# Optimization experiments

Measured on AMD Instinct MI355X. Metric: run time of the kernel, lower is better.

Reference implementation:

```python
import jax, jax.numpy as jnp
import numpy as np

B, N, DIM, H = 8, 1024, 1024, 8
HEAD_DIM = DIM // H
SCALE = HEAD_DIM ** -0.5  # scale_with_head=True


def setup_inputs() -> dict:
    key = jax.random.key(0)
    k1, k2, k3, k4 = jax.random.split(key, 4)
    return {
        "q": jax.random.normal(k1, (B, N, DIM), dtype=jnp.float32),
        "k": jax.random.normal(k2, (B, N, DIM), dtype=jnp.float32),
        "v": jax.random.normal(k3, (B, N, DIM), dtype=jnp.float32),
        "W_out": jax.random.normal(k4, (DIM, DIM), dtype=jnp.float32) * (DIM ** -0.5),
        "b_out": jnp.zeros((DIM,), dtype=jnp.float32),
    }


def reference(q, k, v, W_out, b_out):
    b, n, dim = q.shape
    h, d = H, dim // H
    # b n (h d) -> b h n d
    def split_heads(t):
        return t.reshape(b, n, h, d).transpose(0, 2, 1, 3)
    qh, kh, vh = split_heads(q), split_heads(k), split_heads(v)
    dots = jnp.einsum('bhid,bhjd->bhij', qh, kh) * SCALE
    attn = jax.nn.softmax(dots, axis=-1)
    out = jnp.einsum('bhij,bhjd->bhid', attn, vh)
    out = out.transpose(0, 2, 1, 3).reshape(b, n, dim)  # b h n d -> b n (h d)
    out = out @ W_out.T + b_out  # nn.Linear(dim, dim); dropout p=0 is identity
    return out, attn
```

## Files before the change

### kernel.cpp

```cpp
#include <hip/hip_runtime.h>

typedef __bf16 bf16x8 __attribute__((ext_vector_type(8)));
typedef unsigned short u16x8 __attribute__((ext_vector_type(8)));
typedef unsigned short u16x4 __attribute__((ext_vector_type(4)));
typedef float f32x4 __attribute__((ext_vector_type(4)));

#define B_    8
#define N_    1024
#define DIM_  1024
#define H_    8
#define HD_   128
#define SCALE_ 0.08838834764831845f

__device__ __forceinline__ unsigned short f2bf(float x) {
  unsigned int u = __float_as_uint(x);
  u += 0x7fffu + ((u >> 16) & 1u);
  return (unsigned short)(u >> 16);
}
__device__ __forceinline__ float bf2f(unsigned short h) {
  return __uint_as_float(((unsigned int)h) << 16);
}
__device__ __forceinline__ f32x4 mfma16(u16x8 a, u16x8 b, f32x4 c) {
  return __builtin_amdgcn_mfma_f32_16x16x32_bf16(
      __builtin_bit_cast(bf16x8, a), __builtin_bit_cast(bf16x8, b), c, 0, 0, 0);
}
__device__ __forceinline__ void gl_lds16(const void* g, void* l) {
  __builtin_amdgcn_global_load_lds(
      (const __attribute__((address_space(1))) unsigned int*)g,
      (__attribute__((address_space(3))) unsigned int*)l, 16, 0, 0);
}
#define SBAR() do { asm volatile("" ::: "memory"); __builtin_amdgcn_s_barrier(); \
                    asm volatile("" ::: "memory"); } while (0)
#define LGKM0() do { asm volatile("s_waitcnt lgkmcnt(0)" ::: "memory"); \
                     __builtin_amdgcn_sched_barrier(0); } while (0)
#define VMC(n)  asm volatile("s_waitcnt vmcnt(" #n ")" ::: "memory")

#define WS_KIMG  ((size_t)0)
#define WS_VIMG  ((size_t)32 << 20)
#define WS_WIMG  ((size_t)64 << 20)
#define WS_AOIMG ((size_t)68 << 20)

__global__ __launch_bounds__(256)
void prep_k(const float* __restrict__ gk, char* __restrict__ kimg) {
  const int blk = blockIdx.x;
  const int bh = blk >> 4, it = blk & 15;
  const int bb = bh >> 3, hh = bh & 7;
  const int t = threadIdx.x;
  char* base = kimg + (size_t)bh * 524288 + it * 32768;
  const float* src = gk + ((size_t)bb * N_ + it * 64) * DIM_ + hh * HD_;
  #pragma unroll
  for (int c = 0; c < 8; ++c) {
    const int idx = t + 256 * c;
    const int key = idx >> 5, dq = (idx & 31) * 4;
    f32x4 f = *(const f32x4*)(src + (size_t)key * DIM_ + dq);
    u16x4 h, g;
    #pragma unroll
    for (int j = 0; j < 4; ++j) {
      unsigned short hv = f2bf(f[j]);
      h[j] = hv;
      g[j] = f2bf(f[j] - bf2f(hv));
    }
    const int dh = dq >> 6, dloc = dq & 63;
    const int off = (dloc * 2) ^ ((key & 7) << 4);
    char* dst = base + dh * 16384 + key * 256;
    *(u16x4*)(dst + off) = h;
    *(u16x4*)(dst + 128 + off) = g;
  }
}

__global__ __launch_bounds__(256)
void prep_v(const float* __restrict__ gv, char* __restrict__ vimg) {
  __shared__ float tile[32][132];
  const int blk = blockIdx.x;
  const int bh = blk >> 5, kt = blk & 31;
  const int bb = bh >> 3, hh = bh & 7;
  const int t = threadIdx.x;
  const float* src = gv + ((size_t)bb * N_ + kt * 32) * DIM_ + hh * HD_;
  #pragma unroll
  for (int c = 0; c < 4; ++c) {
    const int idx = t + 256 * c;
    const int key = idx >> 5, dq = (idx & 31) * 4;
    *(f32x4*)&tile[key][dq] = *(const f32x4*)(src + (size_t)key * DIM_ + dq);
  }
  __syncthreads();
  char* base = vimg + (size_t)bh * 524288 + kt * 16384;
  #pragma unroll
  for (int c = 0; c < 2; ++c) {
    const int oc = t + 256 * c;
    const int d = oc >> 2, kc = oc & 3;
    u16x8 h, g;
    #pragma unroll
    for (int j = 0; j < 8; ++j) {
      float x = tile[kc * 8 + j][d];
      unsigned short hv = f2bf(x);
      h[j] = hv;
      g[j] = f2bf(x - bf2f(hv));
    }
    const int off = (d * 64 + kc * 16) ^ ((d & 7) << 4);
    *(u16x8*)(base + off) = h;
    *(u16x8*)(base + 8192 + off) = g;
  }
}

__global__ __launch_bounds__(256)
void prep_w(const float* __restrict__ gw, char* __restrict__ wimg) {
  const int idx = blockIdx.x * 256 + threadIdx.x;
  const int row = idx >> 7, c0 = (idx & 127) * 8;
  const float* s = gw + (size_t)row * DIM_ + c0;
  f32x4 f0 = *(const f32x4*)s;
  f32x4 f1 = *(const f32x4*)(s + 4);
  u16x8 h, g;
  #pragma unroll
  for (int j = 0; j < 8; ++j) {
    float x = j < 4 ? f0[j] : f1[j - 4];
    unsigned short hv = f2bf(x);
    h[j] = hv;
    g[j] = f2bf(x - bf2f(hv));
  }
  const int nt = row >> 6, rl = row & 63;
  const int st = c0 >> 5, kl = c0 & 31;
  char* base = wimg + ((size_t)(nt * 32 + st) * 64 + rl) * 128;
  const int swz = (rl & 7) << 4;
  *(u16x8*)(base + ((kl * 2) ^ swz)) = h;
  *(u16x8*)(base + ((64 + kl * 2) ^ swz)) = g;
}

struct K1Smem {
  unsigned short p[64 * 1024];
  union {
    char kb[2][16384];
    char vt[2][16384];
    struct { char pad[16384]; float partial[4][64]; float rinv[64]; } pp;
  } u;
};

__global__ __launch_bounds__(1024, 4)
void attn_kernel(const float* __restrict__ gq, const char* __restrict__ kimg,
                 const char* __restrict__ vimg, float* __restrict__ gattn,
                 char* __restrict__ aoimg) {
  __shared__ K1Smem sm;
  const int bid = blockIdx.x;
  const int xcd = bid & 7, slot = bid >> 3;
  const int bh = xcd + 8 * (slot >> 4);
  const int qt = slot & 15;
  const int bb = bh >> 3, hh = bh & 7;

  const int tid = threadIdx.x;
  const int wid = tid >> 6, lane = tid & 63;
  const int rg = wid >> 2;
  const int kg = wid & 3;
  const int l15 = lane & 15, l4 = lane >> 4;

  const char* kimg_bh = kimg + (size_t)bh * 524288;
  const char* vimg_bh = vimg + (size_t)bh * 524288;

  auto issueK = [&](int s) {
    const char* src = kimg_bh + s * 16384 + wid * 1024 + lane * 16;
    gl_lds16(src, sm.u.kb[s & 1] + wid * 1024);
  };
  auto issueV = [&](int kt) {
    const char* src = vimg_bh + kt * 16384 + wid * 1024 + lane * 16;
    gl_lds16(src, sm.u.vt[kt & 1] + wid * 1024);
  };

  issueK(0);

  u16x8 qhi[4], qlo[4];
  {
    const int qrow = qt * 64 + rg * 16 + l15;
    const float* qp = gq + ((size_t)bb * N_ + qrow) * DIM_ + hh * HD_;
    #pragma unroll
    for (int t = 0; t < 4; ++t) {
      const int d0 = t * 32 + l4 * 8;
      f32x4 f0 = *(const f32x4*)(qp + d0);
      f32x4 f1 = *(const f32x4*)(qp + d0 + 4);
      #pragma unroll
      for (int j = 0; j < 8; ++j) {
        float x = (j < 4 ? f0[j] : f1[j - 4]) * SCALE_;
        unsigned short hi = f2bf(x);
        qhi[t][j] = hi;
        qlo[t][j] = f2bf(x - bf2f(hi));
      }
    }
  }

  issueK(1);
  VMC(1);
  SBAR();

  float lsum = 0.f;
  const int key16 = kg * 16 + l15;
  const int kswz = (key16 & 7) << 4;
  const char* krow0 = sm.u.kb[0] + key16 * 256;
  const char* krow1 = sm.u.kb[1] + key16 * 256;
  const int prow_i = rg * 16 + l15;
  char* const prow = (char*)sm.p + prow_i * 2048;
  const int pswz = (prow_i & 7) << 4;

  f32x4 a0, a1, a2;
  #pragma unroll 2
  for (int s = 0; s < 32; ++s) {
    const int dh = s & 1;
    if (s >= 1 && s < 31) issueK(s + 1);
    else if (s == 31) issueV(0);
    const char* krow = dh ? krow1 : krow0;
    u16x8 khi[2], klo[2];
    #pragma unroll
    for (int tl = 0; tl < 2; ++tl) {
      const int off = (tl * 64 + l4 * 16) ^ kswz;
      khi[tl] = *(const u16x8*)(krow + off);
      klo[tl] = *(const u16x8*)(krow + 128 + off);
    }
    if (dh == 0) {
      a0 = f32x4{0.f, 0.f, 0.f, 0.f};
      a1 = f32x4{0.f, 0.f, 0.f, 0.f};
      a2 = f32x4{0.f, 0.f, 0.f, 0.f};
    }
    __builtin_amdgcn_s_setprio(1);
    #pragma unroll
    for (int tl = 0; tl < 2; ++tl) {
      const int t = dh * 2 + tl;
      a0 = mfma16(khi[tl], qhi[t], a0);
      a1 = mfma16(klo[tl], qhi[t], a1);
      a2 = mfma16(khi[tl], qlo[t], a2);
    }
    __builtin_amdgcn_s_setprio(0);
    if (dh == 1) {
      const int keyb = ((s >> 1) * 64 + kg * 16 + l4 * 4) * 2;
      u16x4 pk;
      float ls = 0.f;
      #pragma unroll
      for (int r = 0; r < 4; ++r) {
        float sv = (a0[r] + a1[r]) + a2[r];
        sv = fminf(sv, 60.0f);
        float p = __expf(sv);
        ls += p;
        pk[r] = f2bf(p);
      }
      lsum += ls;
      *(u16x4*)(prow + (keyb ^ pswz)) = pk;
    }
    if (s < 31) VMC(0);
    SBAR();
  }

  {
    float s0 = lsum;
    s0 += __shfl_xor(s0, 16);
    s0 += __shfl_xor(s0, 32);
    if (lane < 16) sm.u.pp.partial[kg][rg * 16 + lane] = s0;
  }
  LGKM0();
  SBAR();
  if (tid < 64) {
    float t4 = sm.u.pp.partial[0][tid] + sm.u.pp.partial[1][tid] +
               sm.u.pp.partial[2][tid] + sm.u.pp.partial[3][tid];
    sm.u.pp.rinv[tid] = 1.0f / t4;
  }
  LGKM0();
  SBAR();
  float rvf[4];
  #pragma unroll
  for (int r = 0; r < 4; ++r)
    rvf[r] = sm.u.pp.rinv[rg * 16 + l4 * 4 + r];
  const bool writer = (kg == 0);
  float rvw = 0.f;
  if (writer) rvw = sm.u.pp.rinv[prow_i];
  LGKM0();
  VMC(0);
  SBAR();

  f32x4 oacc[2];
  oacc[0] = f32x4{0.f, 0.f, 0.f, 0.f};
  oacc[1] = f32x4{0.f, 0.f, 0.f, 0.f};

  float* arow = nullptr;
  if (writer)
    arow = gattn + ((size_t)bh * N_ + qt * 64 + prow_i) * N_ + l4 * 8;

  #pragma unroll 2
  for (int kt = 0; kt < 32; ++kt) {
    if (kt < 31) issueV(kt + 1);
    const char* vbase = sm.u.vt[kt & 1];
    u16x8 vh[2], vl[2];
    #pragma unroll
    for (int ct = 0; ct < 2; ++ct) {
      const int d = kg * 32 + ct * 16 + l15;
      const int off = (d * 64 + l4 * 16) ^ ((d & 7) << 4);
      vh[ct] = *(const u16x8*)(vbase + off);
      vl[ct] = *(const u16x8*)(vbase + 8192 + off);
    }
    u16x8 pa = *(const u16x8*)(prow + ((kt * 64 + l4 * 16) ^ pswz));
    __builtin_amdgcn_s_setprio(1);
    #pragma unroll
    for (int ct = 0; ct < 2; ++ct) {
      oacc[ct] = mfma16(pa, vh[ct], oacc[ct]);
      oacc[ct] = mfma16(pa, vl[ct], oacc[ct]);
    }
    __builtin_amdgcn_s_setprio(0);
    if (writer) {
      f32x4 o0, o1;
      o0[0] = bf2f(pa[0]) * rvw; o0[1] = bf2f(pa[1]) * rvw;
      o0[2] = bf2f(pa[2]) * rvw; o0[3] = bf2f(pa[3]) * rvw;
      o1[0] = bf2f(pa[4]) * rvw; o1[1] = bf2f(pa[5]) * rvw;
      o1[2] = bf2f(pa[6]) * rvw; o1[3] = bf2f(pa[7]) * rvw;
      __builtin_nontemporal_store(o0, (f32x4*)(arow + kt * 32));
      __builtin_nontemporal_store(o1, (f32x4*)(arow + kt * 32 + 4));
    }
    LGKM0();
    if (kt < 31) {
      if (writer) { VMC(2); }
      else        { VMC(0); }
    }
    SBAR();
  }

  {
    char* aobase = aoimg + ((size_t)((bb * 16 + qt) * 32 + hh * 4 + kg)) * 8192;
    #pragma unroll
    for (int ct = 0; ct < 2; ++ct) {
      const int colloc = ct * 16 + l15;
      #pragma unroll
      for (int r = 0; r < 4; ++r) {
        const int rl = rg * 16 + l4 * 4 + r;
        const int swz = (rl & 7) << 4;
        float val = oacc[ct][r] * rvf[r];
        unsigned short hv = f2bf(val);
        unsigned short lv = f2bf(val - bf2f(hv));
        char* rp = aobase + rl * 128;
        __builtin_nontemporal_store(hv, (unsigned short*)(rp + ((colloc * 2) ^ swz)));
        __builtin_nontemporal_store(lv, (unsigned short*)(rp + ((64 + colloc * 2) ^ swz)));
      }
    }
  }
}

struct K2Smem {
  char A[2][8192];
  char Bm[2][8192];
};

__global__ __launch_bounds__(512)
void proj_kernel(const char* __restrict__ aoimg, const char* __restrict__ wimg,
                 const float* __restrict__ gbias, float* __restrict__ gout) {
  __shared__ K2Smem sm;
  const int orig = blockIdx.x;
  const int xcd = orig & 7, idx = orig >> 3;
  const int nt = xcd * 2 + (idx >> 7);
  const int mt = idx & 127;
  const int tid = threadIdx.x;
  const int wid = tid >> 6, lane = tid & 63;
  const int wr = wid >> 2, wc = wid & 3;
  const int l15 = lane & 15, l4 = lane >> 4;

  auto issue = [&](int s) {
    const char* sa = aoimg + ((size_t)(mt * 32 + s)) * 8192 + wid * 1024 + lane * 16;
    gl_lds16(sa, sm.A[s & 1] + wid * 1024);
    const char* sb = wimg + ((size_t)(nt * 32 + s)) * 8192 + wid * 1024 + lane * 16;
    gl_lds16(sb, sm.Bm[s & 1] + wid * 1024);
  };

  f32x4 acc[2];
  acc[0] = f32x4{0.f, 0.f, 0.f, 0.f};
  acc[1] = f32x4{0.f, 0.f, 0.f, 0.f};

  issue(0);
  VMC(0);
  SBAR();
  #pragma unroll 2
  for (int s = 0; s < 32; ++s) {
    if (s < 31) issue(s + 1);
    const char* Ab = sm.A[s & 1];
    const char* Bb = sm.Bm[s & 1];
    u16x8 ah[2], al[2], bh, bl;
    #pragma unroll
    for (int t = 0; t < 2; ++t) {
      const int row = wr * 32 + t * 16 + l15;
      const char* rp = Ab + row * 128;
      const int swz = (row & 7) << 4;
      ah[t] = *(const u16x8*)(rp + ((l4 * 16) ^ swz));
      al[t] = *(const u16x8*)(rp + ((64 + l4 * 16) ^ swz));
    }
    {
      const int col = wc * 16 + l15;
      const char* rp = Bb + col * 128;
      const int swz = (col & 7) << 4;
      bh = *(const u16x8*)(rp + ((l4 * 16) ^ swz));
      bl = *(const u16x8*)(rp + ((64 + l4 * 16) ^ swz));
    }
    __builtin_amdgcn_s_setprio(1);
    #pragma unroll
    for (int i = 0; i < 2; ++i) {
      acc[i] = mfma16(ah[i], bh, acc[i]);
      acc[i] = mfma16(ah[i], bl, acc[i]);
      acc[i] = mfma16(al[i], bh, acc[i]);
    }
    __builtin_amdgcn_s_setprio(0);
    LGKM0();
    if (s < 31) VMC(0);
    SBAR();
  }

  const int col = nt * 64 + wc * 16 + l15;
  const float bv = gbias[col];
  #pragma unroll
  for (int i = 0; i < 2; ++i) {
    float* dst = gout + (size_t)(mt * 64 + wr * 32 + i * 16 + l4 * 4) * DIM_ + col;
    #pragma unroll
    for (int r = 0; r < 4; ++r)
      dst[(size_t)r * DIM_] = acc[i][r] + bv;
  }
}

extern "C" void kernel_launch(void* const* d_in, const int* in_sizes, int n_in,
                              void* d_out, int out_size, void* d_ws, size_t ws_size,
                              hipStream_t stream) {
  const float* q    = (const float*)d_in[0];
  const float* k    = (const float*)d_in[1];
  const float* v    = (const float*)d_in[2];
  const float* W    = (const float*)d_in[3];
  const float* bias = (const float*)d_in[4];
  float* out  = (float*)d_out;
  float* attn = out + (size_t)B_ * N_ * DIM_;

  char* ws = (char*)d_ws;
  char* kimg  = ws + WS_KIMG;
  char* vimg  = ws + WS_VIMG;
  char* wimg  = ws + WS_WIMG;
  char* aoimg = ws + WS_AOIMG;

  prep_k<<<64 * 16, 256, 0, stream>>>(k, kimg);
  prep_v<<<64 * 32, 256, 0, stream>>>(v, vimg);
  prep_w<<<512, 256, 0, stream>>>(W, wimg);
  attn_kernel<<<B_ * H_ * (N_ / 64), 1024, 0, stream>>>(q, kimg, vimg, attn, aoimg);
  proj_kernel<<<2048, 512, 0, stream>>>(aoimg, wimg, bias, out);
}
```

Measured before the change: 278.1 us.

## Merge prep kernels, use 32x32 MFMA for PV, enlarge projection tiles

Merges the three prep kernels into one launch. The attention PV phase moves to 32x32x16 MFMA, with waves split across key halves and a cross-wave LDS reduction; the V image layout changes to match. The projection GEMM goes from 64x64 to 128x128 tiles per block with a 4x2 accumulator grid per wave, raising operand reuse and cutting grid size. The costs are more register pressure, an extra barrier and reduction in the attention epilogue, and fewer, larger blocks in the projection.

Result: slower. 317.4 us (+14.1%).

```diff
diff --git a/kernel.cpp b/kernel.cpp
--- a/kernel.cpp
+++ b/kernel.cpp
@@ -4,6 +4,7 @@
 typedef unsigned short u16x8 __attribute__((ext_vector_type(8)));
 typedef unsigned short u16x4 __attribute__((ext_vector_type(4)));
 typedef float f32x4 __attribute__((ext_vector_type(4)));
+typedef float f32x16 __attribute__((ext_vector_type(16)));
 
 #define B_    8
 #define N_    1024
@@ -24,6 +25,10 @@
   return __builtin_amdgcn_mfma_f32_16x16x32_bf16(
       __builtin_bit_cast(bf16x8, a), __builtin_bit_cast(bf16x8, b), c, 0, 0, 0);
 }
+__device__ __forceinline__ f32x16 mfma32(u16x8 a, u16x8 b, f32x16 c) {
+  return __builtin_amdgcn_mfma_f32_32x32x16_bf16(
+      __builtin_bit_cast(bf16x8, a), __builtin_bit_cast(bf16x8, b), c, 0, 0, 0);
+}
 __device__ __forceinline__ void gl_lds16(const void* g, void* l) {
   __builtin_amdgcn_global_load_lds(
       (const __attribute__((address_space(1))) unsigned int*)g,
@@ -41,95 +46,96 @@
 #define WS_AOIMG ((size_t)68 << 20)
 
 __global__ __launch_bounds__(256)
-void prep_k(const float* __restrict__ gk, char* __restrict__ kimg) {
+void prep_all(const float* __restrict__ gk, const float* __restrict__ gv,
+              const float* __restrict__ gw, char* __restrict__ kimg,
+              char* __restrict__ vimg, char* __restrict__ wimg) {
   const int blk = blockIdx.x;
-  const int bh = blk >> 4, it = blk & 15;
-  const int bb = bh >> 3, hh = bh & 7;
   const int t = threadIdx.x;
-  char* base = kimg + (size_t)bh * 524288 + it * 32768;
-  const float* src = gk + ((size_t)bb * N_ + it * 64) * DIM_ + hh * HD_;
-  #pragma unroll
-  for (int c = 0; c < 8; ++c) {
-    const int idx = t + 256 * c;
-    const int key = idx >> 5, dq = (idx & 31) * 4;
-    f32x4 f = *(const f32x4*)(src + (size_t)key * DIM_ + dq);
-    u16x4 h, g;
-    #pragma unroll
-    for (int j = 0; j < 4; ++j) {
-      unsigned short hv = f2bf(f[j]);
-      h[j] = hv;
-      g[j] = f2bf(f[j] - bf2f(hv));
-    }
-    const int dh = dq >> 6, dloc = dq & 63;
-    const int off = (dloc * 2) ^ ((key & 7) << 4);
-    char* dst = base + dh * 16384 + key * 256;
-    *(u16x4*)(dst + off) = h;
-    *(u16x4*)(dst + 128 + off) = g;
-  }
-}
-
-__global__ __launch_bounds__(256)
-void prep_v(const float* __restrict__ gv, char* __restrict__ vimg) {
-  __shared__ float tile[32][132];
-  const int blk = blockIdx.x;
-  const int bh = blk >> 5, kt = blk & 31;
-  const int bb = bh >> 3, hh = bh & 7;
-  const int t = threadIdx.x;
-  const float* src = gv + ((size_t)bb * N_ + kt * 32) * DIM_ + hh * HD_;
-  #pragma unroll
-  for (int c = 0; c < 4; ++c) {
-    const int idx = t + 256 * c;
-    const int key = idx >> 5, dq = (idx & 31) * 4;
-    *(f32x4*)&tile[key][dq] = *(const f32x4*)(src + (size_t)key * DIM_ + dq);
-  }
-  __syncthreads();
-  char* base = vimg + (size_t)bh * 524288 + kt * 16384;
-  #pragma unroll
-  for (int c = 0; c < 2; ++c) {
-    const int oc = t + 256 * c;
-    const int d = oc >> 2, kc = oc & 3;
+  if (blk < 1024) {
+    const int bh = blk >> 4, it = blk & 15;
+    const int bb = bh >> 3, hh = bh & 7;
+    char* base = kimg + (size_t)bh * 524288 + it * 32768;
+    const float* src = gk + ((size_t)bb * N_ + it * 64) * DIM_ + hh * HD_;
+    #pragma unroll
+    for (int c = 0; c < 8; ++c) {
+      const int idx = t + 256 * c;
+      const int key = idx >> 5, dq = (idx & 31) * 4;
+      f32x4 f = *(const f32x4*)(src + (size_t)key * DIM_ + dq);
+      u16x4 h, g;
+      #pragma unroll
+      for (int j = 0; j < 4; ++j) {
+        unsigned short hv = f2bf(f[j]);
+        h[j] = hv;
+        g[j] = f2bf(f[j] - bf2f(hv));
+      }
+      const int dh = dq >> 6, dloc = dq & 63;
+      const int off = (dloc * 2) ^ ((key & 7) << 4);
+      char* dst = base + dh * 16384 + key * 256;
+      *(u16x4*)(dst + off) = h;
+      *(u16x4*)(dst + 128 + off) = g;
+    }
+  } else if (blk < 3072) {
+    __shared__ float tile[32][132];
+    const int b2 = blk - 1024;
+    const int bh = b2 >> 5, kt = b2 & 31;
+    const int bb = bh >> 3, hh = bh & 7;
+    const float* src = gv + ((size_t)bb * N_ + kt * 32) * DIM_ + hh * HD_;
+    #pragma unroll
+    for (int c = 0; c < 4; ++c) {
+      const int idx = t + 256 * c;
+      const int key = idx >> 5, dq = (idx & 31) * 4;
+      *(f32x4*)&tile[key][dq] = *(const f32x4*)(src + (size_t)key * DIM_ + dq);
+    }
+    __syncthreads();
+    char* base = vimg + (size_t)bh * 524288 + kt * 16384;
+    #pragma unroll
+    for (int c = 0; c < 2; ++c) {
+      const int idx = t + 256 * c;
+      const int d = idx >> 2, koct = idx & 3;
+      const int sb = koct >> 1, k8 = (koct & 1) * 8;
+      u16x8 h, g;
+      #pragma unroll
+      for (int j = 0; j < 8; ++j) {
+        float x = tile[sb * 16 + k8 + j][d];
+        unsigned short hv = f2bf(x);
+        h[j] = hv;
+        g[j] = f2bf(x - bf2f(hv));
+      }
+      const int off = d * 32 + ((k8 * 2) ^ ((d & 1) << 4));
+      char* dst = base + sb * 8192;
+      *(u16x8*)(dst + off) = h;
+      *(u16x8*)(dst + 4096 + off) = g;
+    }
+  } else {
+    const int idx = (blk - 3072) * 256 + t;
+    const int n = idx >> 7, k8 = idx & 127;
+    const int k0 = k8 * 8;
+    const float* s = gw + (size_t)n * DIM_ + k0;
+    f32x4 f0 = *(const f32x4*)s;
+    f32x4 f1 = *(const f32x4*)(s + 4);
     u16x8 h, g;
     #pragma unroll
     for (int j = 0; j < 8; ++j) {
-      float x = tile[kc * 8 + j][d];
+      float x = j < 4 ? f0[j] : f1[j - 4];
       unsigned short hv = f2bf(x);
       h[j] = hv;
       g[j] = f2bf(x - bf2f(hv));
     }
-    const int off = (d * 64 + kc * 16) ^ ((d & 7) << 4);
-    *(u16x8*)(base + off) = h;
-    *(u16x8*)(base + 8192 + off) = g;
-  }
-}
-
-__global__ __launch_bounds__(256)
-void prep_w(const float* __restrict__ gw, char* __restrict__ wimg) {
-  const int idx = blockIdx.x * 256 + threadIdx.x;
-  const int row = idx >> 7, c0 = (idx & 127) * 8;
-  const float* s = gw + (size_t)row * DIM_ + c0;
-  f32x4 f0 = *(const f32x4*)s;
-  f32x4 f1 = *(const f32x4*)(s + 4);
-  u16x8 h, g;
-  #pragma unroll
-  for (int j = 0; j < 8; ++j) {
-    float x = j < 4 ? f0[j] : f1[j - 4];
-    unsigned short hv = f2bf(x);
-    h[j] = hv;
-    g[j] = f2bf(x - bf2f(hv));
-  }
-  const int nt = row >> 6, rl = row & 63;
-  const int st = c0 >> 5, kl = c0 & 31;
-  char* base = wimg + ((size_t)(nt * 32 + st) * 64 + rl) * 128;
-  const int swz = (rl & 7) << 4;
-  *(u16x8*)(base + ((kl * 2) ^ swz)) = h;
-  *(u16x8*)(base + ((64 + kl * 2) ^ swz)) = g;
+    const int T = (n >> 7) * 32 + (k0 >> 5);
+    const int rl = n & 127, kl = k0 & 31;
+    char* base = wimg + (size_t)T * 16384 + rl * 128;
+    const int swz = (rl & 7) << 4;
+    *(u16x8*)(base + ((kl * 2) ^ swz)) = h;
+    *(u16x8*)(base + ((64 + kl * 2) ^ swz)) = g;
+  }
 }
 
 struct K1Smem {
   unsigned short p[64 * 1024];
   union {
     char kb[2][16384];
-    char vt[2][16384];
+    char vb[4][8192];
+    char comb[8][4096];
     struct { char pad[16384]; float partial[4][64]; float rinv[64]; } pp;
   } u;
 };
@@ -150,6 +156,10 @@
   const int rg = wid >> 2;
   const int kg = wid & 3;
   const int l15 = lane & 15, l4 = lane >> 4;
+  const int prg = wid >> 3;
+  const int pkg = kg;
+  const int pkh = (wid >> 2) & 1;
+  const int l31 = lane & 31, l5 = lane >> 5;
 
   const char* kimg_bh = kimg + (size_t)bh * 524288;
   const char* vimg_bh = vimg + (size_t)bh * 524288;
@@ -158,9 +168,10 @@
     const char* src = kimg_bh + s * 16384 + wid * 1024 + lane * 16;
     gl_lds16(src, sm.u.kb[s & 1] + wid * 1024);
   };
-  auto issueV = [&](int kt) {
-    const char* src = vimg_bh + kt * 16384 + wid * 1024 + lane * 16;
-    gl_lds16(src, sm.u.vt[kt & 1] + wid * 1024);
+  auto issueVpair = [&](int pairbase) {
+    const int sb = pairbase + (wid >> 3);
+    const char* src = vimg_bh + (size_t)sb * 8192 + (wid & 7) * 1024 + lane * 16;
+    gl_lds16(src, sm.u.vb[sb & 3] + (wid & 7) * 1024);
   };
 
   issueK(0);
@@ -202,7 +213,7 @@
   for (int s = 0; s < 32; ++s) {
     const int dh = s & 1;
     if (s >= 1 && s < 31) issueK(s + 1);
-    else if (s == 31) issueV(0);
+    else if (s == 31) issueVpair(0);
     const char* krow = dh ? krow1 : krow0;
     u16x8 khi[2], klo[2];
     #pragma unroll
@@ -240,7 +251,8 @@
       lsum += ls;
       *(u16x4*)(prow + (keyb ^ pswz)) = pk;
     }
-    if (s < 31) VMC(0);
+    if (s < 31) { VMC(0); }
+    else       { VMC(2); }
     SBAR();
   }
 
@@ -259,156 +271,184 @@
   }
   LGKM0();
   SBAR();
-  float rvf[4];
-  #pragma unroll
-  for (int r = 0; r < 4; ++r)
-    rvf[r] = sm.u.pp.rinv[rg * 16 + l4 * 4 + r];
-  const bool writer = (kg == 0);
-  float rvw = 0.f;
-  if (writer) rvw = sm.u.pp.rinv[prow_i];
+  const float rvw = sm.u.pp.rinv[prg * 32 + l31];
+  float rv16[16];
+  if (pkh == 0) {
+    #pragma unroll
+    for (int r = 0; r < 16; ++r) {
+      const int rowreg = (r & 3) + 8 * (r >> 2) + 4 * l5;
+      rv16[r] = sm.u.pp.rinv[prg * 32 + rowreg];
+    }
+  }
   LGKM0();
   VMC(0);
   SBAR();
 
-  f32x4 oacc[2];
-  oacc[0] = f32x4{0.f, 0.f, 0.f, 0.f};
-  oacc[1] = f32x4{0.f, 0.f, 0.f, 0.f};
-
-  float* arow = nullptr;
-  if (writer)
-    arow = gattn + ((size_t)bh * N_ + qt * 64 + prow_i) * N_ + l4 * 8;
-
-  #pragma unroll 2
-  for (int kt = 0; kt < 32; ++kt) {
-    if (kt < 31) issueV(kt + 1);
-    const char* vbase = sm.u.vt[kt & 1];
-    u16x8 vh[2], vl[2];
-    #pragma unroll
-    for (int ct = 0; ct < 2; ++ct) {
-      const int d = kg * 32 + ct * 16 + l15;
-      const int off = (d * 64 + l4 * 16) ^ ((d & 7) << 4);
-      vh[ct] = *(const u16x8*)(vbase + off);
-      vl[ct] = *(const u16x8*)(vbase + 8192 + off);
-    }
-    u16x8 pa = *(const u16x8*)(prow + ((kt * 64 + l4 * 16) ^ pswz));
+  f32x16 acc = {};
+  const char* pArow = (const char*)sm.p + (prg * 32 + l31) * 2048;
+  const int paswz = ((prg * 32 + l31) & 7) << 4;
+  float* arow = gattn + ((size_t)bh * N_ + qt * 64 + prg * 32 + l31) * N_;
+
+  #pragma unroll 1
+  for (int t = 0; t < 32; ++t) {
+    if (t < 31) issueVpair(2 * (t + 1));
+    const int s = 2 * t + pkh;
+    const char* vbase = sm.u.vb[s & 3];
+    const int d = pkg * 32 + l31;
+    const int voff = d * 32 + ((l5 * 16) ^ ((d & 1) << 4));
+    u16x8 vh = *(const u16x8*)(vbase + voff);
+    u16x8 vl = *(const u16x8*)(vbase + 4096 + voff);
+    u16x8 pa = *(const u16x8*)(pArow + ((s * 32 + l5 * 16) ^ paswz));
     __builtin_amdgcn_s_setprio(1);
-    #pragma unroll
-    for (int ct = 0; ct < 2; ++ct) {
-      oacc[ct] = mfma16(pa, vh[ct], oacc[ct]);
-      oacc[ct] = mfma16(pa, vl[ct], oacc[ct]);
-    }
+    acc = mfma32(pa, vh, acc);
+    acc = mfma32(pa, vl, acc);
     __builtin_amdgcn_s_setprio(0);
-    if (writer) {
+    const bool wr = ((t & 3) == pkg);
+    if (wr) {
       f32x4 o0, o1;
       o0[0] = bf2f(pa[0]) * rvw; o0[1] = bf2f(pa[1]) * rvw;
       o0[2] = bf2f(pa[2]) * rvw; o0[3] = bf2f(pa[3]) * rvw;
       o1[0] = bf2f(pa[4]) * rvw; o1[1] = bf2f(pa[5]) * rvw;
       o1[2] = bf2f(pa[6]) * rvw; o1[3] = bf2f(pa[7]) * rvw;
-      __builtin_nontemporal_store(o0, (f32x4*)(arow + kt * 32));
-      __builtin_nontemporal_store(o1, (f32x4*)(arow + kt * 32 + 4));
+      float* dst = arow + s * 16 + l5 * 8;
+      __builtin_nontemporal_store(o0, (f32x4*)dst);
+      __builtin_nontemporal_store(o1, (f32x4*)(dst + 4));
     }
     LGKM0();
-    if (kt < 31) {
-      if (writer) { VMC(2); }
-      else        { VMC(0); }
+    if (t < 31) {
+      if (wr) { VMC(2); }
+      else    { VMC(0); }
     }
     SBAR();
   }
 
   {
-    char* aobase = aoimg + ((size_t)((bb * 16 + qt) * 32 + hh * 4 + kg)) * 8192;
-    #pragma unroll
-    for (int ct = 0; ct < 2; ++ct) {
-      const int colloc = ct * 16 + l15;
-      #pragma unroll
-      for (int r = 0; r < 4; ++r) {
-        const int rl = rg * 16 + l4 * 4 + r;
+    char* cbase = sm.u.comb[prg * 4 + pkg] + lane * 64;
+    if (pkh == 1) {
+      #pragma unroll
+      for (int q = 0; q < 4; ++q) {
+        f32x4 v = {acc[q * 4], acc[q * 4 + 1], acc[q * 4 + 2], acc[q * 4 + 3]};
+        *(f32x4*)(cbase + q * 16) = v;
+      }
+    }
+    LGKM0();
+    SBAR();
+    if (pkh == 0) {
+      #pragma unroll
+      for (int q = 0; q < 4; ++q) {
+        f32x4 v = *(const f32x4*)(cbase + q * 16);
+        acc[q * 4] += v[0]; acc[q * 4 + 1] += v[1];
+        acc[q * 4 + 2] += v[2]; acc[q * 4 + 3] += v[3];
+      }
+      const int col5 = hh * 4 + pkg;
+      const int mt = bb * 8 + (qt >> 1);
+      char* Tbase = aoimg + ((size_t)(mt * 32 + col5)) * 16384;
+      const int klb = (l31) * 2;
+      #pragma unroll
+      for (int r = 0; r < 16; ++r) {
+        const int rowreg = (r & 3) + 8 * (r >> 2) + 4 * l5;
+        const int rl = (qt & 1) * 64 + prg * 32 + rowreg;
         const int swz = (rl & 7) << 4;
-        float val = oacc[ct][r] * rvf[r];
+        float val = acc[r] * rv16[r];
         unsigned short hv = f2bf(val);
         unsigned short lv = f2bf(val - bf2f(hv));
-        char* rp = aobase + rl * 128;
-        __builtin_nontemporal_store(hv, (unsigned short*)(rp + ((colloc * 2) ^ swz)));
-        __builtin_nontemporal_store(lv, (unsigned short*)(rp + ((64 + colloc * 2) ^ swz)));
+        char* rp = Tbase + rl * 128;
+        __builtin_nontemporal_store(hv, (unsigned short*)(rp + (klb ^ swz)));
+        __builtin_nontemporal_store(lv, (unsigned short*)(rp + ((64 + klb) ^ swz)));
       }
     }
   }
 }
 
 struct K2Smem {
-  char A[2][8192];
-  char Bm[2][8192];
+  char A[2][16384];
+  char Bm[2][16384];
 };
 
-__global__ __launch_bounds__(512)
+__global__ __launch_bounds__(512, 2)
 void proj_kernel(const char* __restrict__ aoimg, const char* __restrict__ wimg,
                  const float* __restrict__ gbias, float* __restrict__ gout) {
   __shared__ K2Smem sm;
-  const int orig = blockIdx.x;
-  const int xcd = orig & 7, idx = orig >> 3;
-  const int nt = xcd * 2 + (idx >> 7);
-  const int mt = idx & 127;
+  const int nt = blockIdx.x & 7;
+  const int mt = blockIdx.x >> 3;
   const int tid = threadIdx.x;
   const int wid = tid >> 6, lane = tid & 63;
   const int wr = wid >> 2, wc = wid & 3;
   const int l15 = lane & 15, l4 = lane >> 4;
 
   auto issue = [&](int s) {
-    const char* sa = aoimg + ((size_t)(mt * 32 + s)) * 8192 + wid * 1024 + lane * 16;
-    gl_lds16(sa, sm.A[s & 1] + wid * 1024);
-    const char* sb = wimg + ((size_t)(nt * 32 + s)) * 8192 + wid * 1024 + lane * 16;
-    gl_lds16(sb, sm.Bm[s & 1] + wid * 1024);
+    const char* sa = aoimg + ((size_t)(mt * 32 + s)) * 16384 + tid * 16;
+    gl_lds16(sa, sm.A[s & 1] + (tid >> 6) * 1024);
+    gl_lds16(sa + 8192, sm.A[s & 1] + 8192 + (tid >> 6) * 1024);
+    const char* sb = wimg + ((size_t)(nt * 32 + s)) * 16384 + tid * 16;
+    gl_lds16(sb, sm.Bm[s & 1] + (tid >> 6) * 1024);
+    gl_lds16(sb + 8192, sm.Bm[s & 1] + 8192 + (tid >> 6) * 1024);
   };
 
-  f32x4 acc[2];
-  acc[0] = f32x4{0.f, 0.f, 0.f, 0.f};
-  acc[1] = f32x4{0.f, 0.f, 0.f, 0.f};
+  f32x4 acc[4][2];
+  #pragma unroll
+  for (int i = 0; i < 4; ++i)
+    #pragma unroll
+    for (int j = 0; j < 2; ++j) acc[i][j] = f32x4{0.f, 0.f, 0.f, 0.f};
 
   issue(0);
   VMC(0);
   SBAR();
-  #pragma unroll 2
+  #pragma unroll 1
   for (int s = 0; s < 32; ++s) {
     if (s < 31) issue(s + 1);
     const char* Ab = sm.A[s & 1];
     const char* Bb = sm.Bm[s & 1];
-    u16x8 ah[2], al[2], bh, bl;
-    #pragma unroll
-    for (int t = 0; t < 2; ++t) {
-      const int row = wr * 32 + t * 16 + l15;
-      const char* rp = Ab + row * 128;
-      const int swz = (row & 7) << 4;
-      ah[t] = *(const u16x8*)(rp + ((l4 * 16) ^ swz));
-      al[t] = *(const u16x8*)(rp + ((64 + l4 * 16) ^ swz));
-    }
-    {
-      const int col = wc * 16 + l15;
-      const char* rp = Bb + col * 128;
-      const int swz = (col & 7) << 4;
-      bh = *(const u16x8*)(rp + ((l4 * 16) ^ swz));
-      bl = *(const u16x8*)(rp + ((64 + l4 * 16) ^ swz));
+    u16x8 ah[4], al[4], bh[2], bl[2];
+    #pragma unroll
+    for (int rt = 0; rt < 4; ++rt) {
+      const int rl = wr * 64 + rt * 16 + l15;
+      const char* rp = Ab + rl * 128;
+      const int swz = (rl & 7) << 4;
+      ah[rt] = *(const u16x8*)(rp + ((l4 * 16) ^ swz));
+      al[rt] = *(const u16x8*)(rp + ((64 + l4 * 16) ^ swz));
+    }
+    #pragma unroll
+    for (int ct = 0; ct < 2; ++ct) {
+      const int cl = wc * 32 + ct * 16 + l15;
+      const char* rp = Bb + cl * 128;
+      const int swz = (cl & 7) << 4;
+      bh[ct] = *(const u16x8*)(rp + ((l4 * 16) ^ swz));
+      bl[ct] = *(const u16x8*)(rp + ((64 + l4 * 16) ^ swz));
     }
     __builtin_amdgcn_s_setprio(1);
     #pragma unroll
-    for (int i = 0; i < 2; ++i) {
-      acc[i] = mfma16(ah[i], bh, acc[i]);
-      acc[i] = mfma16(ah[i], bl, acc[i]);
-      acc[i] = mfma16(al[i], bh, acc[i]);
-    }
+    for (int rt = 0; rt < 4; ++rt)
+      #pragma unroll
+      for (int ct = 0; ct < 2; ++ct)
+        acc[rt][ct] = mfma16(ah[rt], bh[ct], acc[rt][ct]);
+    #pragma unroll
+    for (int rt = 0; rt < 4; ++rt)
+      #pragma unroll
+      for (int ct = 0; ct < 2; ++ct)
+        acc[rt][ct] = mfma16(ah[rt], bl[ct], acc[rt][ct]);
+    #pragma unroll
+    for (int rt = 0; rt < 4; ++rt)
+      #pragma unroll
+      for (int ct = 0; ct < 2; ++ct)
+        acc[rt][ct] = mfma16(al[rt], bh[ct], acc[rt][ct]);
     __builtin_amdgcn_s_setprio(0);
     LGKM0();
     if (s < 31) VMC(0);
     SBAR();
   }
 
-  const int col = nt * 64 + wc * 16 + l15;
-  const float bv = gbias[col];
   #pragma unroll
-  for (int i = 0; i < 2; ++i) {
-    float* dst = gout + (size_t)(mt * 64 + wr * 32 + i * 16 + l4 * 4) * DIM_ + col;
-    #pragma unroll
-    for (int r = 0; r < 4; ++r)
-      dst[(size_t)r * DIM_] = acc[i][r] + bv;
+  for (int ct = 0; ct < 2; ++ct) {
+    const int col = nt * 128 + wc * 32 + ct * 16 + l15;
+    const float bv = gbias[col];
+    #pragma unroll
+    for (int rt = 0; rt < 4; ++rt) {
+      float* dst = gout + (size_t)(mt * 128 + wr * 64 + rt * 16 + l4 * 4) * DIM_ + col;
+      #pragma unroll
+      for (int r = 0; r < 4; ++r)
+        dst[(size_t)r * DIM_] = acc[rt][ct][r] + bv;
+    }
   }
 }
 
@@ -429,9 +469,7 @@
   char* wimg  = ws + WS_WIMG;
   char* aoimg = ws + WS_AOIMG;
 
-  prep_k<<<64 * 16, 256, 0, stream>>>(k, kimg);
-  prep_v<<<64 * 32, 256, 0, stream>>>(v, vimg);
-  prep_w<<<512, 256, 0, stream>>>(W, wimg);
+  prep_all<<<3584, 256, 0, stream>>>(k, v, W, kimg, vimg, wimg);
   attn_kernel<<<B_ * H_ * (N_ / 64), 1024, 0, stream>>>(q, kimg, vimg, attn, aoimg);
-  proj_kernel<<<2048, 512, 0, stream>>>(aoimg, wimg, bias, out);
-}
+  proj_kernel<<<512, 512, 0, stream>>>(aoimg, wimg, bias, out);
+}
```
